# Performance work log

Hardware: AMD Instinct MI355X
Metric: run time of the kernel (lower is better)

## Reference

```python
import jax, jax.numpy as jnp
import numpy as np

B, T, D = 256, 336, 128
H = 1024
N_LABEL, LABEL_CLASS = 24, 1
FORGET_BIAS = 1.0  # TF BasicLSTMCell default


def setup_inputs() -> dict:
    key = jax.random.key(0)
    ks = jax.random.split(key, 8)
    s1 = 1.0 / np.sqrt(D + H)
    s2 = 1.0 / np.sqrt(2 * H)
    sd = 1.0 / np.sqrt(H)
    return {
        "features": jax.random.normal(ks[0], (B, T, D), jnp.float32),
        "labels": jax.random.normal(ks[1], (B, N_LABEL, LABEL_CLASS), jnp.float32),
        "W1": jax.random.normal(ks[2], (D + H, 4 * H), jnp.float32) * s1,
        "b1": jnp.zeros((4 * H,), jnp.float32),
        "W2": jax.random.normal(ks[3], (2 * H, 4 * H), jnp.float32) * s2,
        "b2": jnp.zeros((4 * H,), jnp.float32),
        "Wd": jax.random.normal(ks[4], (H, N_LABEL * LABEL_CLASS), jnp.float32) * sd,
        "bd": jnp.zeros((N_LABEL * LABEL_CLASS,), jnp.float32),
    }


def _lstm_cell(c, h, x, W, b):
    # TF BasicLSTMCell: gates = [x, h] @ W + b, split into i, j, f, o
    z = jnp.concatenate([x, h], axis=-1) @ W + b
    i, j, f, o = jnp.split(z, 4, axis=-1)
    new_c = c * jax.nn.sigmoid(f + FORGET_BIAS) + jax.nn.sigmoid(i) * jnp.tanh(j)
    new_h = jnp.tanh(new_c) * jax.nn.sigmoid(o)
    return new_c, new_h


def reference(features, labels, W1, b1, W2, b2, Wd, bd):
    batch = features.shape[0]
    zeros = jnp.zeros((batch, H), features.dtype)
    init = (zeros, zeros, zeros, zeros)  # c1, h1, c2, h2

    def step(carry, x_t):
        c1, h1, c2, h2 = carry
        c1, h1 = _lstm_cell(c1, h1, x_t, W1, b1)
        c2, h2 = _lstm_cell(c2, h2, h1, W2, b2)
        return (c1, h1, c2, h2), None

    xs = jnp.swapaxes(features, 0, 1)  # [T, B, D]
    (c1, h1, c2, h2), _ = jax.lax.scan(step, init, xs)
    # dense head on last-timestep output of top layer
    pred = (h2 @ Wd + bd).reshape(batch, N_LABEL, LABEL_CLASS)
    loss = jnp.mean(jnp.square(pred - labels))
    return loss
```

## Files before the change

kernel.cpp:

```cpp
#include <hip/hip_runtime.h>

#define TT 336
#define BB 256
#define DD 128
#define HH 1024
#define TD 43008
#define BBHH 262144

#define SSU0 20480u
#define SSU1 32768u
#define LBU1 5242880u

#define ZTS 124

typedef __attribute__((ext_vector_type(8))) short short8;
typedef __attribute__((ext_vector_type(8))) unsigned short ushort8;
typedef __attribute__((ext_vector_type(4))) unsigned short ushort4v;
typedef __attribute__((ext_vector_type(4))) float floatx4;

#define OFF_ZPAD 0u
#define OFF_BAR  4096u
#define OFF_H1   2101248u
#define OFF_H2   3149824u
#define OFF_B1P  4198400u
#define OFF_B2P  4214784u
#define OFF_X    4231168u
#define OFF_BP   26251264u

static __device__ __forceinline__ unsigned short f2bf(float f) {
  unsigned int x = __float_as_uint(f);
  x += 0x7fffu + ((x >> 16) & 1u);
  return (unsigned short)(x >> 16);
}
static __device__ __forceinline__ float bf2f(unsigned short u) {
  return __uint_as_float(((unsigned int)u) << 16);
}
static __device__ __forceinline__ float sigm(float x) {
  return 1.f / (1.f + __expf(-x));
}
static __device__ __forceinline__ float tanh_fast(float x) {
  float ax = fabsf(x);
  float e = __expf(-2.f * ax);
  float t = (1.f - e) / (1.f + e);
  return x < 0.f ? -t : t;
}

#define GLOAD_LDS16(gsrc, ldst)                                              \
  __builtin_amdgcn_global_load_lds(                                          \
      (const __attribute__((address_space(1))) void*)(gsrc),                 \
      (__attribute__((address_space(3))) void*)(ldst), 16, 0, 0)
#define GLOAD_LDS16_DC(gsrc, ldst)                                           \
  __builtin_amdgcn_global_load_lds(                                          \
      (const __attribute__((address_space(1))) void*)(gsrc),                 \
      (__attribute__((address_space(3))) void*)(ldst), 16, 0, 17)

#define ASM_MEMBAR asm volatile("" ::: "memory")

__global__ __launch_bounds__(256) void init_zero(float* out, uint4* span, long n16) {
  long i = (long)blockIdx.x * 256 + threadIdx.x;
  if (i < n16) span[i] = make_uint4(0u, 0u, 0u, 0u);
  if (i == 0) out[0] = 0.f;
}

__global__ __launch_bounds__(256) void feat2bf(const float* __restrict__ in,
                                               unsigned short* __restrict__ out, long nq) {
  long Q = (long)blockIdx.x * 256 + threadIdx.x;
  if (Q >= nq) return;
  int b = (int)(Q / 5376);
  long outQ = (Q & ~7L) | ((Q ^ (long)b) & 7);
  const floatx4* pp = (const floatx4*)(in + Q * 8);
  floatx4 a = pp[0], c = pp[1];
  ushort8 v;
  #pragma unroll
  for (int q = 0; q < 4; ++q) { v[q] = f2bf(a[q]); v[4 + q] = f2bf(c[q]); }
  *(ushort8*)(out + outQ * 8) = v;
}

__global__ __launch_bounds__(256) void bpack(const float* __restrict__ W1,
                                             const float* __restrict__ W2,
                                             unsigned short* __restrict__ out) {
  __shared__ unsigned short tile[64][72];
  int bid = blockIdx.x, t = threadIdx.x;
  int L, tk, tn;
  if (bid < 1280) { L = 0; tk = bid % 20; tn = bid / 20; }
  else            { L = 1; tk = (bid - 1280) % 32; tn = (bid - 1280) / 32; }
  const float* W = L ? W2 : W1;
  int KG = L ? 512 : 320;
  int k0 = tk * 64, n0p = tn * 64;
  int g = k0 / KG;
  int ksg0 = (k0 - g * KG) >> 5;
  int ntile = n0p >> 7, wn = (n0p >> 6) & 1;
  unsigned int SSu = L ? SSU1 : SSU0;
  unsigned int base = (L ? LBU1 : 0u) + ntile * 8u * SSu + (g * 2 + wn) * SSu;

  #pragma unroll
  for (int i = 0; i < 16; ++i) {
    int idx = i * 256 + t;
    int kk = idx >> 6, nn = idx & 63;
    int np = n0p + nn;
    int norig = ((np & 3) << 10) + (np >> 2);
    float v = 0.f;
    if (!(L == 0 && k0 + kk >= 1152)) v = W[(size_t)(k0 + kk) * 4096 + norig];
    tile[kk][nn] = f2bf(v);
  }
  __syncthreads();
  int t64 = t & 63;
  #pragma unroll
  for (int pass = 0; pass < 2; ++pass) {
    int f = (t >> 6) + pass * 4;
    int ksl = f >> 2, ni = f & 3;
    ushort8 v;
    #pragma unroll
    for (int j = 0; j < 8; ++j)
      v[j] = tile[ksl * 32 + ((t64 >> 4) << 3) + j][ni * 16 + (t64 & 15)];
    *(ushort8*)(out + base + (unsigned)((ksg0 + ksl) * 4 + ni) * 512u + t64 * 8) = v;
  }
}

__global__ __launch_bounds__(256) void bias_perm(const float* __restrict__ b1,
                                                 const float* __restrict__ b2,
                                                 float* __restrict__ b1p,
                                                 float* __restrict__ b2p) {
  int idx = blockIdx.x * 256 + threadIdx.x;
  const float* src = (idx < 4096) ? b1 : b2;
  float* dst = (idx < 4096) ? b1p : b2p;
  int n = idx & 4095;
  dst[n] = src[(n & 3) * 1024 + (n >> 2)];
}

__global__ __launch_bounds__(512, 2) void lstm_persist(
    const unsigned short* __restrict__ Xbf,
    unsigned short* __restrict__ h1bufs, unsigned short* __restrict__ h2bufs,
    const unsigned short* __restrict__ Bpack,
    const float* __restrict__ b1p, const float* __restrict__ b2p,
    const unsigned short* __restrict__ zpad,
    unsigned int* __restrict__ bar) {
  __shared__ __align__(16) unsigned short Abuf[4][3][64 * 64];
  __shared__ __align__(16) float zt0[64 * ZTS];
  __shared__ __align__(16) float zt1[64 * ZTS];

  int bid = blockIdx.x;
  int layer = bid >> 7;
  int lid = bid & 127;
  int ntile = (lid & 7) | (((lid >> 5) & 3) << 3);
  int mtile = (lid >> 3) & 3;
  int m0 = mtile * 64;
  int u0 = ntile * 32;
  const int KG = layer ? 512 : 320;
  const int NIT = KG >> 6;

  int tid = threadIdx.x;
  int g = tid >> 7;
  int wn = (tid >> 6) & 1;
  int lane = tid & 63;
  int kgbase = g * KG;

  unsigned int SSu = layer ? SSU1 : SSU0;
  const unsigned short* bwave =
      Bpack + (layer ? LBU1 : 0u) + ntile * 8u * SSu + (unsigned)(g * 2 + wn) * SSu;

  int r = tid >> 3, ug = tid & 7;
  int rgc = m0 + r;
  const float* bp = (layer ? b2p : b1p) + (size_t)(u0 + ug * 4) * 4;
  floatx4 breg[4];
  #pragma unroll
  for (int k = 0; k < 4; ++k) breg[k] = *(const floatx4*)&bp[k * 4];
  floatx4 creg = (floatx4){0.f, 0.f, 0.f, 0.f};

  unsigned int* gctr = bar;
  unsigned int* xctr = bar + 16 * (1 + (bid & 7));

  for (int p = 0; p <= TT; ++p) {
    bool active = layer ? (p >= 1) : (p < TT);
    if (active) {
      const unsigned short* hp1 = h1bufs + (size_t)(p & 1) * BBHH;
      const unsigned short* hp2 = h2bufs + (size_t)(p & 1) * BBHH;

      auto stageA = [&](int buf, int it) {
        int kb = kgbase + (it << 6);
        unsigned short* dst0 = &Abuf[g][buf][0];
        #pragma unroll
        for (int c = 0; c < 4; ++c) {
          int rowbase = c * 16 + wn * 8;
          int rg = m0 + rowbase + (lane >> 3);
          int kq = lane & 7;
          if (layer == 0) {
            if (kb < DD) {
              GLOAD_LDS16(Xbf + (size_t)rg * TD + p * DD + kb + kq * 8,
                          dst0 + rowbase * 64);
            } else if (kb < 1152) {
              GLOAD_LDS16_DC(hp1 + (size_t)rg * HH + (kb - DD) + kq * 8,
                             dst0 + rowbase * 64);
            } else {
              GLOAD_LDS16(zpad + lane * 8, dst0 + rowbase * 64);
            }
          } else {
            if (kb < HH) {
              GLOAD_LDS16_DC(hp1 + (size_t)rg * HH + kb + kq * 8,
                             dst0 + rowbase * 64);
            } else {
              GLOAD_LDS16_DC(hp2 + (size_t)rg * HH + (kb - HH) + kq * 8,
                             dst0 + rowbase * 64);
            }
          }
        }
      };
      auto loadB = [&](ushort8 (&dst)[2][4], int it) {
        #pragma unroll
        for (int ksl = 0; ksl < 2; ++ksl)
          #pragma unroll
          for (int ni = 0; ni < 4; ++ni)
            dst[ksl][ni] =
                *(const ushort8*)(bwave + (unsigned)((it * 2 + ksl) * 4 + ni) * 512u + lane * 8);
      };

      floatx4 acc[4][4];
      #pragma unroll
      for (int i = 0; i < 4; ++i)
        #pragma unroll
        for (int j = 0; j < 4; ++j) acc[i][j] = (floatx4){0.f, 0.f, 0.f, 0.f};

      ushort8 bc[2][4], bn[2][4];

      auto computeIt = [&](int buf, ushort8 (&bb)[2][4]) {
        const unsigned short* Ab = &Abuf[g][buf][0];
        #pragma unroll
        for (int ksl = 0; ksl < 2; ++ksl) {
          int qb = ksl * 4 + (lane >> 4);
          short8 af[4];
          #pragma unroll
          for (int mi = 0; mi < 4; ++mi) {
            int ml = mi * 16 + (lane & 15);
            af[mi] = *(const short8*)&Ab[ml * 64 + ((qb ^ (ml & 7)) << 3)];
          }
          #pragma unroll
          for (int mi = 0; mi < 4; ++mi)
            #pragma unroll
            for (int ni = 0; ni < 4; ++ni)
              acc[mi][ni] = __builtin_amdgcn_mfma_f32_16x16x32_bf16(
                  af[mi], (short8)bb[ksl][ni], acc[mi][ni], 0, 0, 0);
        }
      };

      stageA(0, 0);
      ASM_MEMBAR;
      loadB(bc, 0);
      ASM_MEMBAR;
      stageA(1, 1);
      ASM_MEMBAR;

      for (int it = 0; it < NIT - 1; ++it) {
        asm volatile("s_waitcnt vmcnt(4)" ::: "memory");
        __builtin_amdgcn_s_barrier();
        loadB(bn, it + 1);
        ASM_MEMBAR;
        if (it + 2 < NIT) stageA((it + 2) % 3, it + 2);
        ASM_MEMBAR;
        computeIt(it % 3, bc);
        #pragma unroll
        for (int ksl = 0; ksl < 2; ++ksl)
          #pragma unroll
          for (int ni = 0; ni < 4; ++ni) bc[ksl][ni] = bn[ksl][ni];
      }
      asm volatile("s_waitcnt vmcnt(0)" ::: "memory");
      __builtin_amdgcn_s_barrier();
      computeIt((NIT - 1) % 3, bc);

      float* ztw = (g & 1) ? zt1 : zt0;
      if (g < 2) {
        #pragma unroll
        for (int mi = 0; mi < 4; ++mi)
          #pragma unroll
          for (int ni = 0; ni < 4; ++ni)
            #pragma unroll
            for (int rr = 0; rr < 4; ++rr) {
              int row = mi * 16 + (lane >> 4) * 4 + rr;
              int col = wn * 64 + ni * 16 + (lane & 15);
              ztw[row * ZTS + col] = acc[mi][ni][rr];
            }
      }
      __syncthreads();
      if (g >= 2) {
        #pragma unroll
        for (int mi = 0; mi < 4; ++mi)
          #pragma unroll
          for (int ni = 0; ni < 4; ++ni)
            #pragma unroll
            for (int rr = 0; rr < 4; ++rr) {
              int row = mi * 16 + (lane >> 4) * 4 + rr;
              int col = wn * 64 + ni * 16 + (lane & 15);
              ztw[row * ZTS + col] += acc[mi][ni][rr];
            }
      }
      __syncthreads();

      {
        unsigned short* hn = (layer ? h2bufs : h1bufs) + (size_t)((p + 1) & 1) * BBHH;
        floatx4 cold = creg, cn;
        ushort4v hv;
        #pragma unroll
        for (int k = 0; k < 4; ++k) {
          int cbase = r * ZTS + (ug * 4 + k) * 4;
          floatx4 gt0 = *(const floatx4*)&zt0[cbase];
          floatx4 gt1 = *(const floatx4*)&zt1[cbase];
          floatx4 bb = breg[k];
          float i_ = gt0[0] + gt1[0] + bb[0];
          float j_ = gt0[1] + gt1[1] + bb[1];
          float f_ = gt0[2] + gt1[2] + bb[2] + 1.f;
          float o_ = gt0[3] + gt1[3] + bb[3];
          float nc = cold[k] * sigm(f_) + sigm(i_) * tanh_fast(j_);
          cn[k] = nc;
          hv[k] = f2bf(tanh_fast(nc) * sigm(o_));
        }
        creg = cn;
        int q = (u0 >> 3) + (ug >> 1);
        union { ushort4v v; unsigned long long u; } cu;
        cu.v = hv;
        unsigned long long* hdst = (unsigned long long*)
            &hn[(size_t)rgc * HH + (((q & ~7) | ((q ^ rgc) & 7)) << 3) + (ug & 1) * 4];
        __hip_atomic_store(hdst, cu.u, __ATOMIC_RELAXED, __HIP_MEMORY_SCOPE_AGENT);
      }
    }

    __syncthreads();
    if (tid == 0) {
      __hip_atomic_fetch_add(xctr, 1u, __ATOMIC_RELAXED, __HIP_MEMORY_SCOPE_AGENT);
      if (bid < 8) {
        unsigned int wantx = 32u * (unsigned int)(p + 1);
        while (__hip_atomic_load(xctr, __ATOMIC_RELAXED, __HIP_MEMORY_SCOPE_AGENT) < wantx)
          __builtin_amdgcn_s_sleep(1);
        __hip_atomic_fetch_add(gctr, 1u, __ATOMIC_RELAXED, __HIP_MEMORY_SCOPE_AGENT);
      }
      unsigned int want = 8u * (unsigned int)(p + 1);
      while (__hip_atomic_load(gctr, __ATOMIC_RELAXED, __HIP_MEMORY_SCOPE_AGENT) < want)
        __builtin_amdgcn_s_sleep(1);
    }
    __syncthreads();
  }
}

__global__ __launch_bounds__(64) void head_loss(const unsigned short* __restrict__ h2,
                                                const float* __restrict__ Wd,
                                                const float* __restrict__ bd,
                                                const float* __restrict__ labels,
                                                float* __restrict__ out) {
  int b = blockIdx.x;
  int l = threadIdx.x;
  float pacc[24];
  #pragma unroll
  for (int n = 0; n < 24; ++n) pacc[n] = 0.f;
  for (int k = l; k < HH; k += 64) {
    int ksw = (k & ~63) | ((((k >> 3) ^ b) & 7) << 3) | (k & 7);
    float hv = bf2f(h2[(size_t)b * HH + ksw]);
    const float* wr = Wd + (size_t)k * 24;
    #pragma unroll
    for (int n = 0; n < 24; ++n) pacc[n] += hv * wr[n];
  }
  #pragma unroll
  for (int n = 0; n < 24; ++n) {
    float v = pacc[n];
    for (int off = 32; off > 0; off >>= 1) v += __shfl_down(v, off);
    pacc[n] = v;
  }
  if (l == 0) {
    float s = 0.f;
    #pragma unroll
    for (int n = 0; n < 24; ++n) {
      float pred = pacc[n] + bd[n];
      float d = pred - labels[b * 24 + n];
      s += d * d;
    }
    atomicAdd(out, s * (1.0f / 6144.0f));
  }
}

extern "C" void kernel_launch(void* const* d_in, const int* in_sizes, int n_in,
                              void* d_out, int out_size, void* d_ws, size_t ws_size,
                              hipStream_t stream) {
  const float* features = (const float*)d_in[0];
  const float* labels   = (const float*)d_in[1];
  const float* W1 = (const float*)d_in[2];
  const float* b1 = (const float*)d_in[3];
  const float* W2 = (const float*)d_in[4];
  const float* b2 = (const float*)d_in[5];
  const float* Wd = (const float*)d_in[6];
  const float* bd = (const float*)d_in[7];

  char* ws = (char*)d_ws;
  unsigned short* zpad = (unsigned short*)(ws + OFF_ZPAD);
  unsigned int*   bar  = (unsigned int*)(ws + OFF_BAR);
  unsigned short* h1   = (unsigned short*)(ws + OFF_H1);
  unsigned short* h2   = (unsigned short*)(ws + OFF_H2);
  float*          b1p  = (float*)(ws + OFF_B1P);
  float*          b2p  = (float*)(ws + OFF_B2P);
  unsigned short* Xbf  = (unsigned short*)(ws + OFF_X);
  unsigned short* BP   = (unsigned short*)(ws + OFF_BP);
  float* out = (float*)d_out;

  init_zero<<<1026, 256, 0, stream>>>(out, (uint4*)ws, 262400L);
  feat2bf<<<5376, 256, 0, stream>>>(features, Xbf, 1376256L);
  bpack<<<3328, 256, 0, stream>>>(W1, W2, BP);
  bias_perm<<<32, 256, 0, stream>>>(b1, b2, b1p, b2p);

  lstm_persist<<<256, 512, 0, stream>>>(Xbf, h1, h2, BP, b1p, b2p, zpad, bar);

  head_loss<<<256, 64, 0, stream>>>(h2 + BBHH, Wd, bd, labels, out);
}
```

Baseline: 6.044 ms.

## Replace global grid barrier with per-producer write/read flags in persistent LSTM

Result: slower. 6.447 ms (+6.7%).

```diff
diff --git a/kernel.cpp b/kernel.cpp
--- a/kernel.cpp
+++ b/kernel.cpp
@@ -19,7 +19,8 @@
 typedef __attribute__((ext_vector_type(4))) float floatx4;
 
 #define OFF_ZPAD 0u
-#define OFF_BAR  4096u
+#define OFF_WRF  4096u
+#define OFF_RDF  8192u
 #define OFF_H1   2101248u
 #define OFF_H2   3149824u
 #define OFF_B1P  4198400u
@@ -55,6 +56,11 @@
       (__attribute__((address_space(3))) void*)(ldst), 16, 0, 17)
 
 #define ASM_MEMBAR asm volatile("" ::: "memory")
+
+#define FLAG_ST(ptr, val)                                                    \
+  __hip_atomic_store((ptr), (val), __ATOMIC_RELAXED, __HIP_MEMORY_SCOPE_AGENT)
+#define FLAG_LD(ptr)                                                         \
+  __hip_atomic_load((ptr), __ATOMIC_RELAXED, __HIP_MEMORY_SCOPE_AGENT)
 
 __global__ __launch_bounds__(256) void init_zero(float* out, uint4* span, long n16) {
   long i = (long)blockIdx.x * 256 + threadIdx.x;
@@ -134,7 +140,7 @@
     const unsigned short* __restrict__ Bpack,
     const float* __restrict__ b1p, const float* __restrict__ b2p,
     const unsigned short* __restrict__ zpad,
-    unsigned int* __restrict__ bar) {
+    unsigned int* __restrict__ wrf, unsigned int* __restrict__ rdf) {
   __shared__ __align__(16) unsigned short Abuf[4][3][64 * 64];
   __shared__ __align__(16) float zt0[64 * ZTS];
   __shared__ __align__(16) float zt1[64 * ZTS];
@@ -167,175 +173,190 @@
   for (int k = 0; k < 4; ++k) breg[k] = *(const floatx4*)&bp[k * 4];
   floatx4 creg = (floatx4){0.f, 0.f, 0.f, 0.f};
 
-  unsigned int* gctr = bar;
-  unsigned int* xctr = bar + 16 * (1 + (bid & 7));
+  int fl = tid & 63;
+  int fbid = ((fl >> 5) << 7) | (((fl >> 3) & 3) << 5) | (mtile << 3) | (fl & 7);
 
   for (int p = 0; p <= TT; ++p) {
     bool active = layer ? (p >= 1) : (p < TT);
-    if (active) {
-      const unsigned short* hp1 = h1bufs + (size_t)(p & 1) * BBHH;
-      const unsigned short* hp2 = h2bufs + (size_t)(p & 1) * BBHH;
-
-      auto stageA = [&](int buf, int it) {
-        int kb = kgbase + (it << 6);
-        unsigned short* dst0 = &Abuf[g][buf][0];
-        #pragma unroll
-        for (int c = 0; c < 4; ++c) {
-          int rowbase = c * 16 + wn * 8;
-          int rg = m0 + rowbase + (lane >> 3);
-          int kq = lane & 7;
-          if (layer == 0) {
-            if (kb < DD) {
-              GLOAD_LDS16(Xbf + (size_t)rg * TD + p * DD + kb + kq * 8,
-                          dst0 + rowbase * 64);
-            } else if (kb < 1152) {
-              GLOAD_LDS16_DC(hp1 + (size_t)rg * HH + (kb - DD) + kq * 8,
-                             dst0 + rowbase * 64);
-            } else {
-              GLOAD_LDS16(zpad + lane * 8, dst0 + rowbase * 64);
-            }
+    if (!active) {
+      if (tid == 0) {
+        FLAG_ST(&rdf[bid], (unsigned int)(p + 1));
+        FLAG_ST(&wrf[bid], (unsigned int)(p + 1));
+      }
+      continue;
+    }
+    const unsigned short* hp1 = h1bufs + (size_t)(p & 1) * BBHH;
+    const unsigned short* hp2 = h2bufs + (size_t)(p & 1) * BBHH;
+
+    auto stageA = [&](int buf, int it) {
+      int kb = kgbase + (it << 6);
+      unsigned short* dst0 = &Abuf[g][buf][0];
+      #pragma unroll
+      for (int c = 0; c < 4; ++c) {
+        int rowbase = c * 16 + wn * 8;
+        int rg = m0 + rowbase + (lane >> 3);
+        int kq = lane & 7;
+        if (layer == 0) {
+          if (kb < DD) {
+            GLOAD_LDS16(Xbf + (size_t)rg * TD + p * DD + kb + kq * 8,
+                        dst0 + rowbase * 64);
+          } else if (kb < 1152) {
+            GLOAD_LDS16_DC(hp1 + (size_t)rg * HH + (kb - DD) + kq * 8,
+                           dst0 + rowbase * 64);
           } else {
-            if (kb < HH) {
-              GLOAD_LDS16_DC(hp1 + (size_t)rg * HH + kb + kq * 8,
-                             dst0 + rowbase * 64);
-            } else {
-              GLOAD_LDS16_DC(hp2 + (size_t)rg * HH + (kb - HH) + kq * 8,
-                             dst0 + rowbase * 64);
-            }
+            GLOAD_LDS16(zpad + lane * 8, dst0 + rowbase * 64);
+          }
+        } else {
+          if (kb < HH) {
+            GLOAD_LDS16_DC(hp1 + (size_t)rg * HH + kb + kq * 8,
+                           dst0 + rowbase * 64);
+          } else {
+            GLOAD_LDS16_DC(hp2 + (size_t)rg * HH + (kb - HH) + kq * 8,
+                           dst0 + rowbase * 64);
           }
         }
-      };
-      auto loadB = [&](ushort8 (&dst)[2][4], int it) {
-        #pragma unroll
-        for (int ksl = 0; ksl < 2; ++ksl)
-          #pragma unroll
-          for (int ni = 0; ni < 4; ++ni)
-            dst[ksl][ni] =
-                *(const ushort8*)(bwave + (unsigned)((it * 2 + ksl) * 4 + ni) * 512u + lane * 8);
-      };
-
-      floatx4 acc[4][4];
-      #pragma unroll
-      for (int i = 0; i < 4; ++i)
-        #pragma unroll
-        for (int j = 0; j < 4; ++j) acc[i][j] = (floatx4){0.f, 0.f, 0.f, 0.f};
-
-      ushort8 bc[2][4], bn[2][4];
-
-      auto computeIt = [&](int buf, ushort8 (&bb)[2][4]) {
-        const unsigned short* Ab = &Abuf[g][buf][0];
-        #pragma unroll
-        for (int ksl = 0; ksl < 2; ++ksl) {
-          int qb = ksl * 4 + (lane >> 4);
-          short8 af[4];
-          #pragma unroll
-          for (int mi = 0; mi < 4; ++mi) {
-            int ml = mi * 16 + (lane & 15);
-            af[mi] = *(const short8*)&Ab[ml * 64 + ((qb ^ (ml & 7)) << 3)];
-          }
-          #pragma unroll
-          for (int mi = 0; mi < 4; ++mi)
-            #pragma unroll
-            for (int ni = 0; ni < 4; ++ni)
-              acc[mi][ni] = __builtin_amdgcn_mfma_f32_16x16x32_bf16(
-                  af[mi], (short8)bb[ksl][ni], acc[mi][ni], 0, 0, 0);
+      }
+    };
+    auto loadB = [&](ushort8 (&dst)[2][4], int it) {
+      #pragma unroll
+      for (int ksl = 0; ksl < 2; ++ksl)
+        #pragma unroll
+        for (int ni = 0; ni < 4; ++ni)
+          dst[ksl][ni] =
+              *(const ushort8*)(bwave + (unsigned)((it * 2 + ksl) * 4 + ni) * 512u + lane * 8);
+    };
+
+    floatx4 acc[4][4];
+    #pragma unroll
+    for (int i = 0; i < 4; ++i)
+      #pragma unroll
+      for (int j = 0; j < 4; ++j) acc[i][j] = (floatx4){0.f, 0.f, 0.f, 0.f};
+
+    ushort8 bc[2][4], bn[2][4];
+
+    auto computeIt = [&](int buf, ushort8 (&bb)[2][4]) {
+      const unsigned short* Ab = &Abuf[g][buf][0];
+      #pragma unroll
+      for (int ksl = 0; ksl < 2; ++ksl) {
+        int qb = ksl * 4 + (lane >> 4);
+        short8 af[4];
+        #pragma unroll
+        for (int mi = 0; mi < 4; ++mi) {
+          int ml = mi * 16 + (lane & 15);
+          af[mi] = *(const short8*)&Ab[ml * 64 + ((qb ^ (ml & 7)) << 3)];
         }
-      };
-
-      stageA(0, 0);
-      ASM_MEMBAR;
-      loadB(bc, 0);
-      ASM_MEMBAR;
-      stageA(1, 1);
-      ASM_MEMBAR;
-
-      for (int it = 0; it < NIT - 1; ++it) {
-        asm volatile("s_waitcnt vmcnt(4)" ::: "memory");
-        __builtin_amdgcn_s_barrier();
-        loadB(bn, it + 1);
-        ASM_MEMBAR;
-        if (it + 2 < NIT) stageA((it + 2) % 3, it + 2);
-        ASM_MEMBAR;
-        computeIt(it % 3, bc);
-        #pragma unroll
-        for (int ksl = 0; ksl < 2; ++ksl)
-          #pragma unroll
-          for (int ni = 0; ni < 4; ++ni) bc[ksl][ni] = bn[ksl][ni];
-      }
-      asm volatile("s_waitcnt vmcnt(0)" ::: "memory");
-      __builtin_amdgcn_s_barrier();
-      computeIt((NIT - 1) % 3, bc);
-
-      float* ztw = (g & 1) ? zt1 : zt0;
-      if (g < 2) {
         #pragma unroll
         for (int mi = 0; mi < 4; ++mi)
           #pragma unroll
           for (int ni = 0; ni < 4; ++ni)
-            #pragma unroll
-            for (int rr = 0; rr < 4; ++rr) {
-              int row = mi * 16 + (lane >> 4) * 4 + rr;
-              int col = wn * 64 + ni * 16 + (lane & 15);
-              ztw[row * ZTS + col] = acc[mi][ni][rr];
-            }
+            acc[mi][ni] = __builtin_amdgcn_mfma_f32_16x16x32_bf16(
+                af[mi], (short8)bb[ksl][ni], acc[mi][ni], 0, 0, 0);
       }
-      __syncthreads();
-      if (g >= 2) {
-        #pragma unroll
-        for (int mi = 0; mi < 4; ++mi)
+    };
+
+    loadB(bc, 0);
+    ASM_MEMBAR;
+    bool prestaged = (layer == 0 && g == 0);
+    if (prestaged) { stageA(0, 0); ASM_MEMBAR; stageA(1, 1); ASM_MEMBAR; }
+
+    if (tid < 64) {
+      unsigned int want = (unsigned int)p;
+      bool need = layer ? true : (fl < 32);
+      for (;;) {
+        unsigned int v = need ? FLAG_LD(&wrf[fbid]) : want;
+        if (__ballot(v >= want) == ~0ull) break;
+        __builtin_amdgcn_s_sleep(1);
+      }
+    }
+    __builtin_amdgcn_s_barrier();
+    if (!prestaged) { stageA(0, 0); ASM_MEMBAR; stageA(1, 1); ASM_MEMBAR; }
+
+    for (int it = 0; it < NIT - 1; ++it) {
+      asm volatile("s_waitcnt vmcnt(4)" ::: "memory");
+      __builtin_amdgcn_s_barrier();
+      loadB(bn, it + 1);
+      ASM_MEMBAR;
+      if (it + 2 < NIT) stageA((it + 2) % 3, it + 2);
+      ASM_MEMBAR;
+      computeIt(it % 3, bc);
+      #pragma unroll
+      for (int ksl = 0; ksl < 2; ++ksl)
+        #pragma unroll
+        for (int ni = 0; ni < 4; ++ni) bc[ksl][ni] = bn[ksl][ni];
+    }
+    asm volatile("s_waitcnt vmcnt(0)" ::: "memory");
+    __builtin_amdgcn_s_barrier();
+    computeIt((NIT - 1) % 3, bc);
+
+    float* ztw = (g & 1) ? zt1 : zt0;
+    if (g < 2) {
+      #pragma unroll
+      for (int mi = 0; mi < 4; ++mi)
+        #pragma unroll
+        for (int ni = 0; ni < 4; ++ni)
           #pragma unroll
-          for (int ni = 0; ni < 4; ++ni)
-            #pragma unroll
-            for (int rr = 0; rr < 4; ++rr) {
-              int row = mi * 16 + (lane >> 4) * 4 + rr;
-              int col = wn * 64 + ni * 16 + (lane & 15);
-              ztw[row * ZTS + col] += acc[mi][ni][rr];
-            }
+          for (int rr = 0; rr < 4; ++rr) {
+            int row = mi * 16 + (lane >> 4) * 4 + rr;
+            int col = wn * 64 + ni * 16 + (lane & 15);
+            ztw[row * ZTS + col] = acc[mi][ni][rr];
+          }
+    }
+    __syncthreads();
+    if (tid == 0) FLAG_ST(&rdf[bid], (unsigned int)(p + 1));
+    if (g >= 2) {
+      #pragma unroll
+      for (int mi = 0; mi < 4; ++mi)
+        #pragma unroll
+        for (int ni = 0; ni < 4; ++ni)
+          #pragma unroll
+          for (int rr = 0; rr < 4; ++rr) {
+            int row = mi * 16 + (lane >> 4) * 4 + rr;
+            int col = wn * 64 + ni * 16 + (lane & 15);
+            ztw[row * ZTS + col] += acc[mi][ni][rr];
+          }
+    }
+    __syncthreads();
+
+    unsigned short* hn = (layer ? h2bufs : h1bufs) + (size_t)((p + 1) & 1) * BBHH;
+    floatx4 cold = creg, cn;
+    ushort4v hv;
+    #pragma unroll
+    for (int k = 0; k < 4; ++k) {
+      int cbase = r * ZTS + (ug * 4 + k) * 4;
+      floatx4 gt0 = *(const floatx4*)&zt0[cbase];
+      floatx4 gt1 = *(const floatx4*)&zt1[cbase];
+      floatx4 bb = breg[k];
+      float i_ = gt0[0] + gt1[0] + bb[0];
+      float j_ = gt0[1] + gt1[1] + bb[1];
+      float f_ = gt0[2] + gt1[2] + bb[2] + 1.f;
+      float o_ = gt0[3] + gt1[3] + bb[3];
+      float nc = cold[k] * sigm(f_) + sigm(i_) * tanh_fast(j_);
+      cn[k] = nc;
+      hv[k] = f2bf(tanh_fast(nc) * sigm(o_));
+    }
+    creg = cn;
+
+    if (tid < 64) {
+      unsigned int want = (unsigned int)p;
+      bool need = layer ? (fl >= 32) : true;
+      for (;;) {
+        unsigned int v = need ? FLAG_LD(&rdf[fbid]) : want;
+        if (__ballot(v >= want) == ~0ull) break;
+        __builtin_amdgcn_s_sleep(1);
       }
-      __syncthreads();
-
-      {
-        unsigned short* hn = (layer ? h2bufs : h1bufs) + (size_t)((p + 1) & 1) * BBHH;
-        floatx4 cold = creg, cn;
-        ushort4v hv;
-        #pragma unroll
-        for (int k = 0; k < 4; ++k) {
-          int cbase = r * ZTS + (ug * 4 + k) * 4;
-          floatx4 gt0 = *(const floatx4*)&zt0[cbase];
-          floatx4 gt1 = *(const floatx4*)&zt1[cbase];
-          floatx4 bb = breg[k];
-          float i_ = gt0[0] + gt1[0] + bb[0];
-          float j_ = gt0[1] + gt1[1] + bb[1];
-          float f_ = gt0[2] + gt1[2] + bb[2] + 1.f;
-          float o_ = gt0[3] + gt1[3] + bb[3];
-          float nc = cold[k] * sigm(f_) + sigm(i_) * tanh_fast(j_);
-          cn[k] = nc;
-          hv[k] = f2bf(tanh_fast(nc) * sigm(o_));
-        }
-        creg = cn;
-        int q = (u0 >> 3) + (ug >> 1);
-        union { ushort4v v; unsigned long long u; } cu;
-        cu.v = hv;
-        unsigned long long* hdst = (unsigned long long*)
-            &hn[(size_t)rgc * HH + (((q & ~7) | ((q ^ rgc) & 7)) << 3) + (ug & 1) * 4];
-        __hip_atomic_store(hdst, cu.u, __ATOMIC_RELAXED, __HIP_MEMORY_SCOPE_AGENT);
-      }
-    }
-
+    }
+    __builtin_amdgcn_s_barrier();
+
+    {
+      int q = (u0 >> 3) + (ug >> 1);
+      union { ushort4v v; unsigned long long u; } cu;
+      cu.v = hv;
+      unsigned long long* hdst = (unsigned long long*)
+          &hn[(size_t)rgc * HH + (((q & ~7) | ((q ^ rgc) & 7)) << 3) + (ug & 1) * 4];
+      __hip_atomic_store(hdst, cu.u, __ATOMIC_RELAXED, __HIP_MEMORY_SCOPE_AGENT);
+    }
     __syncthreads();
-    if (tid == 0) {
-      __hip_atomic_fetch_add(xctr, 1u, __ATOMIC_RELAXED, __HIP_MEMORY_SCOPE_AGENT);
-      if (bid < 8) {
-        unsigned int wantx = 32u * (unsigned int)(p + 1);
-        while (__hip_atomic_load(xctr, __ATOMIC_RELAXED, __HIP_MEMORY_SCOPE_AGENT) < wantx)
-          __builtin_amdgcn_s_sleep(1);
-        __hip_atomic_fetch_add(gctr, 1u, __ATOMIC_RELAXED, __HIP_MEMORY_SCOPE_AGENT);
-      }
-      unsigned int want = 8u * (unsigned int)(p + 1);
-      while (__hip_atomic_load(gctr, __ATOMIC_RELAXED, __HIP_MEMORY_SCOPE_AGENT) < want)
-        __builtin_amdgcn_s_sleep(1);
-    }
-    __syncthreads();
+    if (tid == 0) FLAG_ST(&wrf[bid], (unsigned int)(p + 1));
   }
 }
 
@@ -388,7 +409,8 @@
 
   char* ws = (char*)d_ws;
   unsigned short* zpad = (unsigned short*)(ws + OFF_ZPAD);
-  unsigned int*   bar  = (unsigned int*)(ws + OFF_BAR);
+  unsigned int*   wrfp = (unsigned int*)(ws + OFF_WRF);
+  unsigned int*   rdfp = (unsigned int*)(ws + OFF_RDF);
   unsigned short* h1   = (unsigned short*)(ws + OFF_H1);
   unsigned short* h2   = (unsigned short*)(ws + OFF_H2);
   float*          b1p  = (float*)(ws + OFF_B1P);
@@ -402,7 +424,8 @@
   bpack<<<3328, 256, 0, stream>>>(W1, W2, BP);
   bias_perm<<<32, 256, 0, stream>>>(b1, b2, b1p, b2p);
 
-  lstm_persist<<<256, 512, 0, stream>>>(Xbf, h1, h2, BP, b1p, b2p, zpad, bar);
+  lstm_persist<<<256, 512, 0, stream>>>(Xbf, h1, h2, BP, b1p, b2p, zpad,
+                                        wrfp, rdfp);
 
   head_loss<<<256, 64, 0, stream>>>(h2 + BBHH, Wd, bd, labels, out);
 }
```

## Prefetch weight fragments across the grid barrier with triple-buffered B registers

Applied to the files above, without the earlier changes.

Measured after the change: 15.04 ms. 149% more time.

```diff
diff --git a/kernel.cpp b/kernel.cpp
--- a/kernel.cpp
+++ b/kernel.cpp
@@ -146,14 +146,13 @@
   int mtile = (lid >> 3) & 3;
   int m0 = mtile * 64;
   int u0 = ntile * 32;
-  const int KG = layer ? 512 : 320;
-  const int NIT = KG >> 6;
+  const int NIT = layer ? 8 : 5;
 
   int tid = threadIdx.x;
   int g = tid >> 7;
   int wn = (tid >> 6) & 1;
   int lane = tid & 63;
-  int kgbase = g * KG;
+  int kgbase = g * (layer ? 512 : 320);
 
   unsigned int SSu = layer ? SSU1 : SSU0;
   const unsigned short* bwave =
@@ -169,6 +168,21 @@
 
   unsigned int* gctr = bar;
   unsigned int* xctr = bar + 16 * (1 + (bid & 7));
+
+  ushort8 bR[3][2][4];
+  auto loadBinto = [&](ushort8 (&dst)[2][4], int it) {
+    #pragma unroll
+    for (int ksl = 0; ksl < 2; ++ksl)
+      #pragma unroll
+      for (int ni = 0; ni < 4; ++ni)
+        dst[ksl][ni] =
+            *(const ushort8*)(bwave + (unsigned)((it * 2 + ksl) * 4 + ni) * 512u + lane * 8);
+  };
+
+  loadBinto(bR[0], 0);
+  ASM_MEMBAR;
+  loadBinto(bR[1], 1);
+  ASM_MEMBAR;
 
   for (int p = 0; p <= TT; ++p) {
     bool active = layer ? (p >= 1) : (p < TT);
@@ -205,22 +219,12 @@
           }
         }
       };
-      auto loadB = [&](ushort8 (&dst)[2][4], int it) {
-        #pragma unroll
-        for (int ksl = 0; ksl < 2; ++ksl)
-          #pragma unroll
-          for (int ni = 0; ni < 4; ++ni)
-            dst[ksl][ni] =
-                *(const ushort8*)(bwave + (unsigned)((it * 2 + ksl) * 4 + ni) * 512u + lane * 8);
-      };
 
       floatx4 acc[4][4];
       #pragma unroll
       for (int i = 0; i < 4; ++i)
         #pragma unroll
         for (int j = 0; j < 4; ++j) acc[i][j] = (floatx4){0.f, 0.f, 0.f, 0.f};
-
-      ushort8 bc[2][4], bn[2][4];
 
       auto computeIt = [&](int buf, ushort8 (&bb)[2][4]) {
         const unsigned short* Ab = &Abuf[g][buf][0];
@@ -244,27 +248,31 @@
 
       stageA(0, 0);
       ASM_MEMBAR;
-      loadB(bc, 0);
-      ASM_MEMBAR;
       stageA(1, 1);
       ASM_MEMBAR;
 
-      for (int it = 0; it < NIT - 1; ++it) {
-        asm volatile("s_waitcnt vmcnt(4)" ::: "memory");
-        __builtin_amdgcn_s_barrier();
-        loadB(bn, it + 1);
-        ASM_MEMBAR;
-        if (it + 2 < NIT) stageA((it + 2) % 3, it + 2);
-        ASM_MEMBAR;
-        computeIt(it % 3, bc);
-        #pragma unroll
-        for (int ksl = 0; ksl < 2; ++ksl)
-          #pragma unroll
-          for (int ni = 0; ni < 4; ++ni) bc[ksl][ni] = bn[ksl][ni];
+#define KLOOP(NITL)                                                          \
+      _Pragma("unroll")                                                      \
+      for (int it = 0; it < (NITL); ++it) {                                  \
+        if (it == 0) {                                                       \
+          asm volatile("s_waitcnt vmcnt(4)" ::: "memory");                   \
+        } else if (it < (NITL) - 1) {                                        \
+          asm volatile("s_waitcnt vmcnt(12)" ::: "memory");                  \
+        } else {                                                             \
+          asm volatile("s_waitcnt vmcnt(0)" ::: "memory");                   \
+        }                                                                    \
+        __builtin_amdgcn_s_barrier();                                        \
+        if (it + 2 < (NITL)) {                                               \
+          loadBinto(bR[(it + 2) % 3], it + 2);                               \
+          ASM_MEMBAR;                                                        \
+          stageA((it + 2) % 3, it + 2);                                      \
+          ASM_MEMBAR;                                                        \
+        }                                                                    \
+        computeIt(it % 3, bR[it % 3]);                                       \
       }
-      asm volatile("s_waitcnt vmcnt(0)" ::: "memory");
-      __builtin_amdgcn_s_barrier();
-      computeIt((NIT - 1) % 3, bc);
+
+      if (layer == 0) { KLOOP(5) } else { KLOOP(8) }
+#undef KLOOP
 
       float* ztw = (g & 1) ? zt1 : zt0;
       if (g < 2) {
@@ -320,9 +328,21 @@
             &hn[(size_t)rgc * HH + (((q & ~7) | ((q ^ rgc) & 7)) << 3) + (ug & 1) * 4];
         __hip_atomic_store(hdst, cu.u, __ATOMIC_RELAXED, __HIP_MEMORY_SCOPE_AGENT);
       }
+      ASM_MEMBAR;
+
+      loadBinto(bR[0], 0);
+      ASM_MEMBAR;
+      loadBinto(bR[1], 1);
+      ASM_MEMBAR;
+      asm volatile("s_waitcnt vmcnt(16)" ::: "memory");
+    } else {
+      loadBinto(bR[0], 0);
+      ASM_MEMBAR;
+      loadBinto(bR[1], 1);
+      ASM_MEMBAR;
     }
 
-    __syncthreads();
+    __builtin_amdgcn_s_barrier();
     if (tid == 0) {
       __hip_atomic_fetch_add(xctr, 1u, __ATOMIC_RELAXED, __HIP_MEMORY_SCOPE_AGENT);
       if (bid < 8) {
@@ -335,7 +355,8 @@
       while (__hip_atomic_load(gctr, __ATOMIC_RELAXED, __HIP_MEMORY_SCOPE_AGENT) < want)
         __builtin_amdgcn_s_sleep(1);
     }
-    __syncthreads();
+    __builtin_amdgcn_s_barrier();
+    ASM_MEMBAR;
   }
 }
 
```
